# Kernel optimization log

Hardware: AMD Instinct MI355X
Metric: run time of the kernel (lower is better)

## Reference

```python
import jax, jax.numpy as jnp
import numpy as np

D_MODEL = 2048
NUM_HEADS = 16
HEAD_DIM = D_MODEL // NUM_HEADS
SCALE = 1.0 / np.sqrt(HEAD_DIM).astype(np.float32)
NEG_INF = -1e9


def setup_inputs() -> dict:
    key = jax.random.key(0)
    ks = jax.random.split(key, 10)
    B, S = 2, 2048
    x = jax.random.normal(ks[0], (B, S, D_MODEL), dtype=jnp.float32)
    # causal lower-triangular mask, broadcastable over (B, H)
    causal_mask = jnp.tril(jnp.ones((S, S), dtype=jnp.int32))[None, None]
    init = 1.0 / np.sqrt(D_MODEL)
    def lin(kw, kb):
        W = jax.random.uniform(kw, (D_MODEL, D_MODEL), jnp.float32, -init, init)
        b = jax.random.uniform(kb, (D_MODEL,), jnp.float32, -init, init)
        return W, b
    Wq, bq = lin(ks[1], ks[2])
    Wk, bk = lin(ks[3], ks[4])
    Wv, bv = lin(ks[5], ks[6])
    Wo, bo = lin(ks[7], ks[8])
    return {"x": x, "causal_mask": causal_mask,
            "Wq": Wq, "bq": bq, "Wk": Wk, "bk": bk,
            "Wv": Wv, "bv": bv, "Wo": Wo, "bo": bo}


def reference(x, causal_mask, Wq, bq, Wk, bk, Wv, bv, Wo, bo):
    B, S, _ = x.shape
    def proj(W, b):
        # torch Linear: x @ W.T + b -> (B, H, S, Dh)
        y = jnp.einsum('bsd,ed->bse', x, W) + b
        return y.reshape(B, S, NUM_HEADS, HEAD_DIM).transpose(0, 2, 1, 3)
    q = proj(Wq, bq)
    k = proj(Wk, bk)
    v = proj(Wv, bv)
    # apply_rope is a no-op stub in the source; q, k unchanged.
    scores = jnp.einsum('bhqd,bhkd->bhqk', q, k) * SCALE
    scores = jnp.where(causal_mask == 0, NEG_INF, scores)
    attn = jax.nn.softmax(scores, axis=-1)
    out = jnp.einsum('bhqk,bhkd->bhqd', attn, v)
    out = out.transpose(0, 2, 1, 3).reshape(B, S, D_MODEL)
    return jnp.einsum('bsd,ed->bse', out, Wo) + bo
```

## Files before the change

kernel.cpp:

```cpp
#include <hip/hip_runtime.h>
#include <hip/hip_bf16.h>
#include <stdint.h>
#include <stddef.h>

typedef __bf16 bf16_t;
typedef __bf16 bf16x4_t __attribute__((ext_vector_type(4)));
typedef __bf16 bf16x8_t __attribute__((ext_vector_type(8)));
typedef float f32x4 __attribute__((ext_vector_type(4)));

#define D_MODEL 2048
#define NHEADS 16
#define HDIM 128
#define SEQ 2048
#define BATCH 2
#define MTOT (BATCH * SEQ)
#define SCALE_F 0.08838834764831845f
#define LOG2E 1.4426950408889634f
#define QSCALE (SCALE_F * LOG2E)

#define AS1 __attribute__((address_space(1)))
#define AS3 __attribute__((address_space(3)))

__device__ __forceinline__ void load_lds16(const bf16_t* g, bf16_t* l) {
  __builtin_amdgcn_global_load_lds((AS1 void*)(g), (AS3 void*)(l), 16, 0, 0);
}

__global__ void cast_kernel(const float* __restrict__ src, bf16_t* __restrict__ dst, int n4) {
  int i = blockIdx.x * blockDim.x + threadIdx.x;
  if (i < n4) {
    float4 v = ((const float4*)src)[i];
    bf16x4_t o;
    o.x = (bf16_t)v.x; o.y = (bf16_t)v.y; o.z = (bf16_t)v.z; o.w = (bf16_t)v.w;
    ((bf16x4_t*)dst)[i] = o;
  }
}

__global__ void cast4_kernel(const float* __restrict__ s0, const float* __restrict__ s1,
                             const float* __restrict__ s2, const float* __restrict__ s3,
                             bf16_t* __restrict__ dst, int n4) {
  int i = blockIdx.x * blockDim.x + threadIdx.x;
  int y = blockIdx.y;
  if (i < n4) {
    const float* src = (y == 0) ? s0 : (y == 1) ? s1 : (y == 2) ? s2 : s3;
    float4 v = ((const float4*)src)[i];
    bf16x4_t o;
    o.x = (bf16_t)v.x; o.y = (bf16_t)v.y; o.z = (bf16_t)v.z; o.w = (bf16_t)v.w;
    ((bf16x4_t*)(dst + (size_t)y * D_MODEL * D_MODEL / 4 * 4))[i] = o;
  }
}

__global__ __launch_bounds__(256) void gemm_fused(
    const bf16_t* __restrict__ A, const bf16_t* __restrict__ Bm, int mode,
    const float* __restrict__ bias0, const float* __restrict__ bias1,
    const float* __restrict__ bias2,
    bf16_t* __restrict__ Qo, bf16_t* __restrict__ Ko, bf16_t* __restrict__ Vto,
    float* __restrict__ Out) {
  const int K = 2048;
  __shared__ __align__(16) bf16_t lA[128 * 64];
  __shared__ __align__(16) bf16_t lB[128 * 64];
  const int m0 = blockIdx.x * 128;
  const int n0 = blockIdx.y * 128;
  const int t = threadIdx.x;
  const int w = t >> 6, lane = t & 63;
  const int wm = w & 1, wn = w >> 1;
  const int la = lane & 15, lb = lane >> 4;

  f32x4 acc[4][4];
  f32x4 zero = {0.f, 0.f, 0.f, 0.f};
#pragma unroll
  for (int i = 0; i < 4; i++)
#pragma unroll
    for (int j = 0; j < 4; j++) acc[i][j] = zero;

  const int row0 = t >> 3, cc = t & 7;
  const int ccs = cc ^ (row0 & 7);
  const bf16_t* gA = A + (size_t)(m0 + row0) * K + ccs * 8;
  const bf16_t* gB = Bm + (size_t)(n0 + row0) * K + ccs * 8;
  bf16_t* sA = lA + t * 8;
  bf16_t* sB = lB + t * 8;

  for (int k0 = 0; k0 < K; k0 += 64) {
    __syncthreads();
#pragma unroll
    for (int i = 0; i < 4; i++)
      load_lds16(gA + k0 + (size_t)(32 * i) * K, sA + 2048 * i);
#pragma unroll
    for (int i = 0; i < 4; i++)
      load_lds16(gB + k0 + (size_t)(32 * i) * K, sB + 2048 * i);
    __syncthreads();
#pragma unroll
    for (int ks = 0; ks < 2; ks++) {
      bf16x8_t af[4], bfr[4];
#pragma unroll
      for (int mt = 0; mt < 4; mt++) {
        int row = wm * 64 + mt * 16 + la;
        af[mt] = *(const bf16x8_t*)(lA + row * 64 + (((ks * 4 + lb) ^ (la & 7)) * 8));
      }
#pragma unroll
      for (int nt = 0; nt < 4; nt++) {
        int row = wn * 64 + nt * 16 + la;
        bfr[nt] = *(const bf16x8_t*)(lB + row * 64 + (((ks * 4 + lb) ^ (la & 7)) * 8));
      }
#pragma unroll
      for (int mt = 0; mt < 4; mt++)
#pragma unroll
        for (int nt = 0; nt < 4; nt++)
          acc[mt][nt] = __builtin_amdgcn_mfma_f32_16x16x32_bf16(af[mt], bfr[nt], acc[mt][nt], 0, 0, 0);
    }
  }

  if (mode == 0) {
#pragma unroll
    for (int mt = 0; mt < 4; mt++) {
#pragma unroll
      for (int nt = 0; nt < 4; nt++) {
        int m = m0 + wm * 64 + mt * 16 + lb * 4;
        int n = n0 + wn * 64 + nt * 16 + la;
        int b = m >> 11, s = m & 2047;
        int which = n >> 11, hd = n & 2047;
        int h = hd >> 7, d = hd & 127;
        float bv = (which == 0 ? bias0 : which == 1 ? bias1 : bias2)[hd];
        f32x4 v = acc[mt][nt];
        if (which == 2) {
          bf16_t* dst = Vto + ((size_t)(b * NHEADS + h) * HDIM + d) * SEQ + s;
          bf16x4_t pk;
          pk.x = (bf16_t)(v.x + bv); pk.y = (bf16_t)(v.y + bv);
          pk.z = (bf16_t)(v.z + bv); pk.w = (bf16_t)(v.w + bv);
          *(bf16x4_t*)dst = pk;
        } else {
          float sc = (which == 0) ? QSCALE : 1.0f;
          bf16_t* dst = (which == 0 ? Qo : Ko) + ((size_t)(b * NHEADS + h) * SEQ + s) * HDIM + d;
          dst[0]        = (bf16_t)((v.x + bv) * sc);
          dst[HDIM]     = (bf16_t)((v.y + bv) * sc);
          dst[2 * HDIM] = (bf16_t)((v.z + bv) * sc);
          dst[3 * HDIM] = (bf16_t)((v.w + bv) * sc);
        }
      }
    }
  } else {
#pragma unroll
    for (int mt = 0; mt < 4; mt++) {
#pragma unroll
      for (int nt = 0; nt < 4; nt++) {
        int m = m0 + wm * 64 + mt * 16 + lb * 4;
        int n = n0 + wn * 64 + nt * 16 + la;
        float bv = bias0[n];
        f32x4 v = acc[mt][nt];
        float* dst = Out + (size_t)m * D_MODEL + n;
        dst[0]           = v.x + bv;
        dst[D_MODEL]     = v.y + bv;
        dst[2 * D_MODEL] = v.z + bv;
        dst[3 * D_MODEL] = v.w + bv;
      }
    }
  }
}

__global__ __launch_bounds__(256, 3) void flash_attn(
    const bf16_t* __restrict__ Q, const bf16_t* __restrict__ Kg,
    const bf16_t* __restrict__ Vt, bf16_t* __restrict__ O,
    bf16_t* __restrict__ PO, float* __restrict__ ML) {
  __shared__ __align__(16) bf16_t lK[64 * 128];
  __shared__ __align__(16) bf16_t lV[128 * 64];
  __shared__ __align__(16) bf16_t lP[128 * 72];
  const int g = blockIdx.x;
  const int piece = g >> 5, bh = g & 31;
  int qt, kt0, kt1, half;
  bool partial;
  if (piece < 16) {
    qt = 8 + (piece >> 1); half = piece & 1; partial = true;
    kt0 = half ? (qt + 1) : 0;
    kt1 = half ? (2 * qt + 2) : (qt + 1);
  } else {
    qt = piece - 16; half = 0; partial = false;
    kt0 = 0; kt1 = 2 * qt + 2;
  }
  const int q0 = qt * 128;
  const int t = threadIdx.x;
  const int w = t >> 6, lane = t & 63;
  const int la = lane & 15, lb = lane >> 4;
  const int qloc = w * 32 + la;

  const bf16_t* Qb = Q + (size_t)bh * SEQ * HDIM;
  const bf16_t* Kb = Kg + (size_t)bh * SEQ * HDIM;
  const bf16_t* Vb = Vt + (size_t)bh * HDIM * SEQ;

  bf16x8_t qf[2][4];
#pragma unroll
  for (int mt = 0; mt < 2; mt++)
#pragma unroll
    for (int ks = 0; ks < 4; ks++)
      qf[mt][ks] = *(const bf16x8_t*)(Qb + (size_t)(q0 + qloc + mt * 16) * HDIM + ks * 32 + lb * 8);

  f32x4 oacc[2][8];
  float mr[2] = {-3.0e38f, -3.0e38f}, lr[2] = {0.f, 0.f};
  f32x4 zero = {0.f, 0.f, 0.f, 0.f};
#pragma unroll
  for (int mt = 0; mt < 2; mt++)
#pragma unroll
    for (int dt = 0; dt < 8; dt++) oacc[mt][dt] = zero;

  for (int kt = kt0; kt < kt1; kt++) {
    const int j0 = kt * 64;
    __syncthreads();
#pragma unroll
    for (int i = 0; i < 4; i++) {
      int slot = t + 256 * i;
      int j = slot >> 4, cc = slot & 15;
      load_lds16(Kb + (size_t)(j0 + j) * HDIM + ((cc ^ (j & 15)) * 8), lK + slot * 8);
    }
#pragma unroll
    for (int i = 0; i < 4; i++) {
      int slot = t + 256 * i;
      int d = slot >> 3, jc = slot & 7;
      load_lds16(Vb + (size_t)d * SEQ + j0 + ((jc ^ (d & 7)) * 8), lV + slot * 8);
    }
    __syncthreads();

    f32x4 st[4][2];
#pragma unroll
    for (int nt = 0; nt < 4; nt++)
#pragma unroll
      for (int mt = 0; mt < 2; mt++) st[nt][mt] = zero;
#pragma unroll
    for (int ks = 0; ks < 4; ks++) {
#pragma unroll
      for (int nt = 0; nt < 4; nt++) {
        int j = nt * 16 + la;
        int cc = (lb + 4 * ks) ^ (j & 15);
        bf16x8_t kf = *(const bf16x8_t*)(lK + j * 128 + cc * 8);
#pragma unroll
        for (int mt = 0; mt < 2; mt++)
          st[nt][mt] = __builtin_amdgcn_mfma_f32_16x16x32_bf16(kf, qf[mt][ks], st[nt][mt], 0, 0, 0);
      }
    }

    const bool dm = (j0 + 64 > q0);
#pragma unroll
    for (int mt = 0; mt < 2; mt++) {
      int qg = q0 + qloc + mt * 16;
      if (dm) {
#pragma unroll
        for (int nt = 0; nt < 4; nt++)
#pragma unroll
          for (int r = 0; r < 4; r++)
            if (j0 + nt * 16 + lb * 4 + r > qg) st[nt][mt][r] = -3.0e38f;
      }
      float tm = -3.0e38f;
#pragma unroll
      for (int nt = 0; nt < 4; nt++)
#pragma unroll
        for (int r = 0; r < 4; r++) tm = fmaxf(tm, st[nt][mt][r]);
      tm = fmaxf(tm, __shfl_xor(tm, 16));
      tm = fmaxf(tm, __shfl_xor(tm, 32));
      float mnew = fmaxf(mr[mt], tm);
      float alpha = exp2f(mr[mt] - mnew);
      mr[mt] = mnew;
      lr[mt] *= alpha;
#pragma unroll
      for (int dt = 0; dt < 8; dt++) oacc[mt][dt] *= alpha;
      float s = 0.f;
#pragma unroll
      for (int nt = 0; nt < 4; nt++) {
        f32x4 p;
#pragma unroll
        for (int r = 0; r < 4; r++) {
          p[r] = exp2f(st[nt][mt][r] - mnew);
          s += p[r];
        }
        bf16x4_t pk;
        pk.x = (bf16_t)p[0]; pk.y = (bf16_t)p[1]; pk.z = (bf16_t)p[2]; pk.w = (bf16_t)p[3];
        *(bf16x4_t*)(lP + (qloc + mt * 16) * 72 + nt * 16 + lb * 4) = pk;
      }
      s += __shfl_xor(s, 16);
      s += __shfl_xor(s, 32);
      lr[mt] += s;
    }

    bf16x8_t pf[2][2];
#pragma unroll
    for (int mt = 0; mt < 2; mt++)
#pragma unroll
      for (int ks = 0; ks < 2; ks++)
        pf[mt][ks] = *(const bf16x8_t*)(lP + (qloc + mt * 16) * 72 + ks * 32 + lb * 8);
#pragma unroll
    for (int ks = 0; ks < 2; ks++) {
#pragma unroll
      for (int dt = 0; dt < 8; dt++) {
        int d = dt * 16 + la;
        int jc = (lb + 4 * ks) ^ (d & 7);
        bf16x8_t vf = *(const bf16x8_t*)(lV + d * 64 + jc * 8);
#pragma unroll
        for (int mt = 0; mt < 2; mt++)
          oacc[mt][dt] = __builtin_amdgcn_mfma_f32_16x16x32_bf16(vf, pf[mt][ks], oacc[mt][dt], 0, 0, 0);
      }
    }
  }

  if (!partial) {
    const int b = bh >> 4, h = bh & 15;
#pragma unroll
    for (int mt = 0; mt < 2; mt++) {
      float inv = 1.0f / lr[mt];
      int q = q0 + qloc + mt * 16;
      bf16_t* dst = O + ((size_t)b * SEQ + q) * D_MODEL + h * HDIM + lb * 4;
#pragma unroll
      for (int dt = 0; dt < 8; dt++) {
        f32x4 v = oacc[mt][dt];
        bf16x4_t pk;
        pk.x = (bf16_t)(v[0] * inv); pk.y = (bf16_t)(v[1] * inv);
        pk.z = (bf16_t)(v[2] * inv); pk.w = (bf16_t)(v[3] * inv);
        *(bf16x4_t*)(dst + dt * 16) = pk;
      }
    }
  } else {
    const int slot = ((qt - 8) * 32 + bh) * 2 + half;
    bf16_t* pob = PO + (size_t)slot * 128 * 128;
#pragma unroll
    for (int mt = 0; mt < 2; mt++) {
      int q = qloc + mt * 16;
      bf16_t* dst = pob + (size_t)q * 128 + lb * 4;
#pragma unroll
      for (int dt = 0; dt < 8; dt++) {
        f32x4 v = oacc[mt][dt];
        bf16x4_t pk;
        pk.x = (bf16_t)v[0]; pk.y = (bf16_t)v[1];
        pk.z = (bf16_t)v[2]; pk.w = (bf16_t)v[3];
        *(bf16x4_t*)(dst + dt * 16) = pk;
      }
      if (lb == 0) {
        float2 ml = make_float2(mr[mt], lr[mt]);
        *(float2*)(ML + ((size_t)slot * 128 + q) * 2) = ml;
      }
    }
  }
}

__global__ void merge_kernel(const bf16_t* __restrict__ PO, const float* __restrict__ ML,
                             bf16_t* __restrict__ O) {
  const int qti = blockIdx.x >> 5, bh = blockIdx.x & 31;
  const int qt = 8 + qti;
  const int t = threadIdx.x;
  const int q = t >> 1, dh = (t & 1) * 64;
  const size_t s1 = ((size_t)(qti * 32 + bh)) * 2;
  const float* ml1 = ML + (s1 * 128 + q) * 2;
  const float* ml2 = ML + ((s1 + 1) * 128 + q) * 2;
  float m1 = ml1[0], l1 = ml1[1], m2 = ml2[0], l2 = ml2[1];
  float m = fmaxf(m1, m2);
  float w1 = exp2f(m1 - m), w2 = exp2f(m2 - m);
  float inv = 1.0f / (w1 * l1 + w2 * l2);
  w1 *= inv; w2 *= inv;
  const bf16_t* p1 = PO + (s1 * 128 + q) * 128 + dh;
  const bf16_t* p2 = PO + ((s1 + 1) * 128 + q) * 128 + dh;
  const int b = bh >> 4, h = bh & 15;
  bf16_t* dst = O + ((size_t)b * SEQ + qt * 128 + q) * D_MODEL + h * HDIM + dh;
#pragma unroll
  for (int i = 0; i < 8; i++) {
    bf16x8_t a = ((const bf16x8_t*)p1)[i];
    bf16x8_t c = ((const bf16x8_t*)p2)[i];
    bf16x8_t o;
#pragma unroll
    for (int e = 0; e < 8; e++)
      o[e] = (bf16_t)(w1 * (float)a[e] + w2 * (float)c[e]);
    ((bf16x8_t*)dst)[i] = o;
  }
}

extern "C" void kernel_launch(void* const* d_in, const int* in_sizes, int n_in,
                              void* d_out, int out_size, void* d_ws, size_t ws_size,
                              hipStream_t stream) {
  (void)in_sizes; (void)n_in; (void)out_size; (void)ws_size;
  const float* x  = (const float*)d_in[0];
  const float* Wq = (const float*)d_in[2];
  const float* bq = (const float*)d_in[3];
  const float* Wk = (const float*)d_in[4];
  const float* bk = (const float*)d_in[5];
  const float* Wv = (const float*)d_in[6];
  const float* bv = (const float*)d_in[7];
  const float* Wo = (const float*)d_in[8];
  const float* bo = (const float*)d_in[9];
  float* out = (float*)d_out;

  const size_t NBF = (size_t)MTOT * D_MODEL * sizeof(bf16_t);
  const size_t WBF = (size_t)D_MODEL * D_MODEL * sizeof(bf16_t);
  char* p = (char*)d_ws;
  bf16_t* xb   = (bf16_t*)p; p += NBF;
  bf16_t* Wcat = (bf16_t*)p; p += 4 * WBF;
  bf16_t* Qb   = (bf16_t*)p; p += NBF;
  bf16_t* Kb   = (bf16_t*)p; p += NBF;
  bf16_t* Vtb  = (bf16_t*)p; p += NBF;
  bf16_t* Wob  = Wcat + (size_t)3 * D_MODEL * D_MODEL;
  bf16_t* Ob   = xb;
  bf16_t* PO = Wcat;
  float*  ML = (float*)(Wcat + (size_t)512 * 128 * 128);

  const int WN4 = D_MODEL * D_MODEL / 4;
  const int XN4 = MTOT * D_MODEL / 4;
  cast_kernel<<<XN4 / 256, 256, 0, stream>>>(x, xb, XN4);
  cast4_kernel<<<dim3(WN4 / 256, 4), 256, 0, stream>>>(Wq, Wk, Wv, Wo, Wcat, WN4);

  gemm_fused<<<dim3(MTOT / 128, 6144 / 128), 256, 0, stream>>>(
      xb, Wcat, 0, bq, bk, bv, Qb, Kb, Vtb, nullptr);

  flash_attn<<<dim3(768), 256, 0, stream>>>(Qb, Kb, Vtb, Ob, PO, ML);
  merge_kernel<<<dim3(256), 256, 0, stream>>>(PO, ML, Ob);

  gemm_fused<<<dim3(MTOT / 128, D_MODEL / 128), 256, 0, stream>>>(
      Ob, Wob, 1, bo, nullptr, nullptr, nullptr, nullptr, nullptr, out);
}
```

Measured before the change: 447.3 us.

## Double-buffer K/V tiles at 32 keys and pair causal work per block

The flash attention kernel now uses 32-key tiles and double-buffers K and V in shared memory, issuing the next tile's async global-to-LDS loads before computing on the current one. Work is rebalanced so that each block processes either one split half of a long query tile or a short query tile paired with the second half of a long one. This drops the grid from 768 to 512 blocks with more even per-block causal work. The intent is to hide load latency and reduce tail imbalance. The cost is extra barriers per key and a different LDS swizzle for V, and the initial max changes to -1e30.

```diff
diff --git a/kernel.cpp b/kernel.cpp
--- a/kernel.cpp
+++ b/kernel.cpp
@@ -17,6 +17,9 @@
 #define SCALE_F 0.08838834764831845f
 #define LOG2E 1.4426950408889634f
 #define QSCALE (SCALE_F * LOG2E)
+#define KT 32
+#define NEGI -3.0e38f
+#define MINIT -1.0e30f
 
 #define AS1 __attribute__((address_space(1)))
 #define AS3 __attribute__((address_space(3)))
@@ -160,22 +163,11 @@
     const bf16_t* __restrict__ Q, const bf16_t* __restrict__ Kg,
     const bf16_t* __restrict__ Vt, bf16_t* __restrict__ O,
     bf16_t* __restrict__ PO, float* __restrict__ ML) {
-  __shared__ __align__(16) bf16_t lK[64 * 128];
-  __shared__ __align__(16) bf16_t lV[128 * 64];
-  __shared__ __align__(16) bf16_t lP[128 * 72];
+  __shared__ __align__(16) bf16_t lK[2][KT * 128];
+  __shared__ __align__(16) bf16_t lV[2][128 * KT];
+  __shared__ __align__(16) bf16_t lP[128 * 40];
   const int g = blockIdx.x;
-  const int piece = g >> 5, bh = g & 31;
-  int qt, kt0, kt1, half;
-  bool partial;
-  if (piece < 16) {
-    qt = 8 + (piece >> 1); half = piece & 1; partial = true;
-    kt0 = half ? (qt + 1) : 0;
-    kt1 = half ? (2 * qt + 2) : (qt + 1);
-  } else {
-    qt = piece - 16; half = 0; partial = false;
-    kt0 = 0; kt1 = 2 * qt + 2;
-  }
-  const int q0 = qt * 128;
+  const int bh = g & 31, idx = g >> 5;
   const int t = threadIdx.x;
   const int w = t >> 6, lane = t & 63;
   const int la = lane & 15, lb = lane >> 4;
@@ -184,153 +176,192 @@
   const bf16_t* Qb = Q + (size_t)bh * SEQ * HDIM;
   const bf16_t* Kb = Kg + (size_t)bh * SEQ * HDIM;
   const bf16_t* Vb = Vt + (size_t)bh * HDIM * SEQ;
-
-  bf16x8_t qf[2][4];
-#pragma unroll
-  for (int mt = 0; mt < 2; mt++)
-#pragma unroll
-    for (int ks = 0; ks < 4; ks++)
-      qf[mt][ks] = *(const bf16x8_t*)(Qb + (size_t)(q0 + qloc + mt * 16) * HDIM + ks * 32 + lb * 8);
-
-  f32x4 oacc[2][8];
-  float mr[2] = {-3.0e38f, -3.0e38f}, lr[2] = {0.f, 0.f};
-  f32x4 zero = {0.f, 0.f, 0.f, 0.f};
-#pragma unroll
-  for (int mt = 0; mt < 2; mt++)
-#pragma unroll
-    for (int dt = 0; dt < 8; dt++) oacc[mt][dt] = zero;
-
-  for (int kt = kt0; kt < kt1; kt++) {
-    const int j0 = kt * 64;
+  const int b = bh >> 4, h = bh & 15;
+
+  int nph, qts[2], k0s[2], k1s[2], slots[2];
+  bool parts[2];
+  if (idx < 8) {
+    nph = 1; qts[0] = 8 + idx; k0s[0] = 0; k1s[0] = 34;
+    parts[0] = true; slots[0] = (idx * 32 + bh) * 2;
+  } else {
+    int qtA = idx - 8;
+    nph = 2;
+    qts[0] = qtA; k0s[0] = 0; k1s[0] = 4 * qtA + 4; parts[0] = false; slots[0] = 0;
+    qts[1] = 15 - qtA; k0s[1] = 34; k1s[1] = 64 - 4 * qtA;
+    parts[1] = true; slots[1] = ((7 - qtA) * 32 + bh) * 2 + 1;
+  }
+
+  const int kj = t >> 4, kcc = t & 15;
+  const int vd = t >> 2, vjc = t & 3;
+
+  for (int ph = 0; ph < nph; ph++) {
+    const int qt = qts[ph], kt0 = k0s[ph], kt1 = k1s[ph];
+    const int q0 = qt * 128;
+
+    bf16x8_t qf[2][4];
+#pragma unroll
+    for (int mt = 0; mt < 2; mt++)
+#pragma unroll
+      for (int ks = 0; ks < 4; ks++)
+        qf[mt][ks] = *(const bf16x8_t*)(Qb + (size_t)(q0 + qloc + mt * 16) * HDIM + ks * 32 + lb * 8);
+
+    f32x4 oacc[2][8];
+    float mr[2] = {MINIT, MINIT}, lr[2] = {0.f, 0.f};
+    f32x4 zero = {0.f, 0.f, 0.f, 0.f};
+#pragma unroll
+    for (int mt = 0; mt < 2; mt++)
+#pragma unroll
+      for (int dt = 0; dt < 8; dt++) oacc[mt][dt] = zero;
+
     __syncthreads();
-#pragma unroll
-    for (int i = 0; i < 4; i++) {
-      int slot = t + 256 * i;
-      int j = slot >> 4, cc = slot & 15;
-      load_lds16(Kb + (size_t)(j0 + j) * HDIM + ((cc ^ (j & 15)) * 8), lK + slot * 8);
-    }
-#pragma unroll
-    for (int i = 0; i < 4; i++) {
-      int slot = t + 256 * i;
-      int d = slot >> 3, jc = slot & 7;
-      load_lds16(Vb + (size_t)d * SEQ + j0 + ((jc ^ (d & 7)) * 8), lV + slot * 8);
-    }
-    __syncthreads();
-
-    f32x4 st[4][2];
-#pragma unroll
-    for (int nt = 0; nt < 4; nt++)
-#pragma unroll
-      for (int mt = 0; mt < 2; mt++) st[nt][mt] = zero;
-#pragma unroll
-    for (int ks = 0; ks < 4; ks++) {
-#pragma unroll
-      for (int nt = 0; nt < 4; nt++) {
-        int j = nt * 16 + la;
-        int cc = (lb + 4 * ks) ^ (j & 15);
-        bf16x8_t kf = *(const bf16x8_t*)(lK + j * 128 + cc * 8);
-#pragma unroll
-        for (int mt = 0; mt < 2; mt++)
-          st[nt][mt] = __builtin_amdgcn_mfma_f32_16x16x32_bf16(kf, qf[mt][ks], st[nt][mt], 0, 0, 0);
-      }
-    }
-
-    const bool dm = (j0 + 64 > q0);
-#pragma unroll
-    for (int mt = 0; mt < 2; mt++) {
-      int qg = q0 + qloc + mt * 16;
-      if (dm) {
-#pragma unroll
-        for (int nt = 0; nt < 4; nt++)
-#pragma unroll
-          for (int r = 0; r < 4; r++)
-            if (j0 + nt * 16 + lb * 4 + r > qg) st[nt][mt][r] = -3.0e38f;
-      }
-      float tm = -3.0e38f;
-#pragma unroll
-      for (int nt = 0; nt < 4; nt++)
-#pragma unroll
-        for (int r = 0; r < 4; r++) tm = fmaxf(tm, st[nt][mt][r]);
-      tm = fmaxf(tm, __shfl_xor(tm, 16));
-      tm = fmaxf(tm, __shfl_xor(tm, 32));
-      float mnew = fmaxf(mr[mt], tm);
-      float alpha = exp2f(mr[mt] - mnew);
-      mr[mt] = mnew;
-      lr[mt] *= alpha;
-#pragma unroll
-      for (int dt = 0; dt < 8; dt++) oacc[mt][dt] *= alpha;
-      float s = 0.f;
-#pragma unroll
-      for (int nt = 0; nt < 4; nt++) {
-        f32x4 p;
-#pragma unroll
-        for (int r = 0; r < 4; r++) {
-          p[r] = exp2f(st[nt][mt][r] - mnew);
-          s += p[r];
-        }
-        bf16x4_t pk;
-        pk.x = (bf16_t)p[0]; pk.y = (bf16_t)p[1]; pk.z = (bf16_t)p[2]; pk.w = (bf16_t)p[3];
-        *(bf16x4_t*)(lP + (qloc + mt * 16) * 72 + nt * 16 + lb * 4) = pk;
-      }
-      s += __shfl_xor(s, 16);
-      s += __shfl_xor(s, 32);
-      lr[mt] += s;
-    }
-
-    bf16x8_t pf[2][2];
-#pragma unroll
-    for (int mt = 0; mt < 2; mt++)
-#pragma unroll
-      for (int ks = 0; ks < 2; ks++)
-        pf[mt][ks] = *(const bf16x8_t*)(lP + (qloc + mt * 16) * 72 + ks * 32 + lb * 8);
-#pragma unroll
-    for (int ks = 0; ks < 2; ks++) {
+    {
+      const int j0 = kt0 * KT;
+      int buf = kt0 & 1;
+#pragma unroll
+      for (int i = 0; i < 2; i++) {
+        int j = kj + 16 * i;
+        load_lds16(Kb + (size_t)(j0 + j) * HDIM + (((kcc ^ (j & 15))) * 8),
+                   lK[buf] + (t + 256 * i) * 8);
+      }
+#pragma unroll
+      for (int i = 0; i < 2; i++) {
+        int d = vd + 64 * i;
+        load_lds16(Vb + (size_t)d * SEQ + j0 + (((vjc ^ ((d & 3) ^ ((d >> 2) & 3)))) * 8),
+                   lV[buf] + (t + 256 * i) * 8);
+      }
+    }
+
+    for (int kt = kt0; kt < kt1; kt++) {
+      const int j0 = kt * KT;
+      const int cur = kt & 1;
+      __syncthreads();
+
+      if (kt + 1 < kt1) {
+        const int jn = (kt + 1) * KT;
+        const int nb = cur ^ 1;
+#pragma unroll
+        for (int i = 0; i < 2; i++) {
+          int j = kj + 16 * i;
+          load_lds16(Kb + (size_t)(jn + j) * HDIM + (((kcc ^ (j & 15))) * 8),
+                     lK[nb] + (t + 256 * i) * 8);
+        }
+#pragma unroll
+        for (int i = 0; i < 2; i++) {
+          int d = vd + 64 * i;
+          load_lds16(Vb + (size_t)d * SEQ + jn + (((vjc ^ ((d & 3) ^ ((d >> 2) & 3)))) * 8),
+                     lV[nb] + (t + 256 * i) * 8);
+        }
+      }
+
+      f32x4 st[2][2];
+#pragma unroll
+      for (int nt = 0; nt < 2; nt++)
+#pragma unroll
+        for (int mt = 0; mt < 2; mt++) st[nt][mt] = zero;
+#pragma unroll
+      for (int ks = 0; ks < 4; ks++) {
+#pragma unroll
+        for (int nt = 0; nt < 2; nt++) {
+          int j = nt * 16 + la;
+          int ck = (ks * 4 + lb) ^ (j & 15);
+          bf16x8_t kf = *(const bf16x8_t*)(lK[cur] + j * 128 + ck * 8);
+#pragma unroll
+          for (int mt = 0; mt < 2; mt++)
+            st[nt][mt] = __builtin_amdgcn_mfma_f32_16x16x32_bf16(kf, qf[mt][ks], st[nt][mt], 0, 0, 0);
+        }
+      }
+
+      const bool dm = (j0 + KT > q0);
+#pragma unroll
+      for (int mt = 0; mt < 2; mt++) {
+        int qg = q0 + qloc + mt * 16;
+        if (dm) {
+#pragma unroll
+          for (int nt = 0; nt < 2; nt++)
+#pragma unroll
+            for (int r = 0; r < 4; r++)
+              if (j0 + nt * 16 + lb * 4 + r > qg) st[nt][mt][r] = NEGI;
+        }
+        float tm = NEGI;
+#pragma unroll
+        for (int nt = 0; nt < 2; nt++)
+#pragma unroll
+          for (int r = 0; r < 4; r++) tm = fmaxf(tm, st[nt][mt][r]);
+        tm = fmaxf(tm, __shfl_xor(tm, 16));
+        tm = fmaxf(tm, __shfl_xor(tm, 32));
+        float mnew = fmaxf(mr[mt], tm);
+        float alpha = exp2f(mr[mt] - mnew);
+        mr[mt] = mnew;
+        lr[mt] *= alpha;
+#pragma unroll
+        for (int dt = 0; dt < 8; dt++) oacc[mt][dt] *= alpha;
+        float s = 0.f;
+#pragma unroll
+        for (int nt = 0; nt < 2; nt++) {
+          f32x4 p;
+#pragma unroll
+          for (int r = 0; r < 4; r++) {
+            p[r] = exp2f(st[nt][mt][r] - mnew);
+            s += p[r];
+          }
+          bf16x4_t pk;
+          pk.x = (bf16_t)p[0]; pk.y = (bf16_t)p[1]; pk.z = (bf16_t)p[2]; pk.w = (bf16_t)p[3];
+          *(bf16x4_t*)(lP + (qloc + mt * 16) * 40 + nt * 16 + lb * 4) = pk;
+        }
+        s += __shfl_xor(s, 16);
+        s += __shfl_xor(s, 32);
+        lr[mt] += s;
+      }
+
+      bf16x8_t pf[2];
+#pragma unroll
+      for (int mt = 0; mt < 2; mt++)
+        pf[mt] = *(const bf16x8_t*)(lP + (w * 32 + mt * 16 + la) * 40 + lb * 8);
 #pragma unroll
       for (int dt = 0; dt < 8; dt++) {
         int d = dt * 16 + la;
-        int jc = (lb + 4 * ks) ^ (d & 7);
-        bf16x8_t vf = *(const bf16x8_t*)(lV + d * 64 + jc * 8);
+        int jc = lb ^ ((d & 3) ^ ((d >> 2) & 3));
+        bf16x8_t vf = *(const bf16x8_t*)(lV[cur] + d * 32 + jc * 8);
 #pragma unroll
         for (int mt = 0; mt < 2; mt++)
-          oacc[mt][dt] = __builtin_amdgcn_mfma_f32_16x16x32_bf16(vf, pf[mt][ks], oacc[mt][dt], 0, 0, 0);
-      }
-    }
-  }
-
-  if (!partial) {
-    const int b = bh >> 4, h = bh & 15;
-#pragma unroll
-    for (int mt = 0; mt < 2; mt++) {
-      float inv = 1.0f / lr[mt];
-      int q = q0 + qloc + mt * 16;
-      bf16_t* dst = O + ((size_t)b * SEQ + q) * D_MODEL + h * HDIM + lb * 4;
-#pragma unroll
-      for (int dt = 0; dt < 8; dt++) {
-        f32x4 v = oacc[mt][dt];
-        bf16x4_t pk;
-        pk.x = (bf16_t)(v[0] * inv); pk.y = (bf16_t)(v[1] * inv);
-        pk.z = (bf16_t)(v[2] * inv); pk.w = (bf16_t)(v[3] * inv);
-        *(bf16x4_t*)(dst + dt * 16) = pk;
-      }
-    }
-  } else {
-    const int slot = ((qt - 8) * 32 + bh) * 2 + half;
-    bf16_t* pob = PO + (size_t)slot * 128 * 128;
-#pragma unroll
-    for (int mt = 0; mt < 2; mt++) {
-      int q = qloc + mt * 16;
-      bf16_t* dst = pob + (size_t)q * 128 + lb * 4;
-#pragma unroll
-      for (int dt = 0; dt < 8; dt++) {
-        f32x4 v = oacc[mt][dt];
-        bf16x4_t pk;
-        pk.x = (bf16_t)v[0]; pk.y = (bf16_t)v[1];
-        pk.z = (bf16_t)v[2]; pk.w = (bf16_t)v[3];
-        *(bf16x4_t*)(dst + dt * 16) = pk;
-      }
-      if (lb == 0) {
-        float2 ml = make_float2(mr[mt], lr[mt]);
-        *(float2*)(ML + ((size_t)slot * 128 + q) * 2) = ml;
+          oacc[mt][dt] = __builtin_amdgcn_mfma_f32_16x16x32_bf16(vf, pf[mt], oacc[mt][dt], 0, 0, 0);
+      }
+    }
+
+    if (!parts[ph]) {
+#pragma unroll
+      for (int mt = 0; mt < 2; mt++) {
+        float inv = 1.0f / lr[mt];
+        int q = q0 + qloc + mt * 16;
+        bf16_t* dst = O + ((size_t)b * SEQ + q) * D_MODEL + h * HDIM + lb * 4;
+#pragma unroll
+        for (int dt = 0; dt < 8; dt++) {
+          f32x4 v = oacc[mt][dt];
+          bf16x4_t pk;
+          pk.x = (bf16_t)(v[0] * inv); pk.y = (bf16_t)(v[1] * inv);
+          pk.z = (bf16_t)(v[2] * inv); pk.w = (bf16_t)(v[3] * inv);
+          *(bf16x4_t*)(dst + dt * 16) = pk;
+        }
+      }
+    } else {
+      const int slot = slots[ph];
+      bf16_t* pob = PO + (size_t)slot * 128 * 128;
+#pragma unroll
+      for (int mt = 0; mt < 2; mt++) {
+        int q = qloc + mt * 16;
+        bf16_t* dst = pob + (size_t)q * 128 + lb * 4;
+#pragma unroll
+        for (int dt = 0; dt < 8; dt++) {
+          f32x4 v = oacc[mt][dt];
+          bf16x4_t pk;
+          pk.x = (bf16_t)v[0]; pk.y = (bf16_t)v[1];
+          pk.z = (bf16_t)v[2]; pk.w = (bf16_t)v[3];
+          *(bf16x4_t*)(dst + dt * 16) = pk;
+        }
+        if (lb == 0) {
+          float2 ml = make_float2(mr[mt], lr[mt]);
+          *(float2*)(ML + ((size_t)slot * 128 + q) * 2) = ml;
+        }
       }
     }
   }
@@ -402,7 +433,7 @@
   gemm_fused<<<dim3(MTOT / 128, 6144 / 128), 256, 0, stream>>>(
       xb, Wcat, 0, bq, bk, bv, Qb, Kb, Vtb, nullptr);
 
-  flash_attn<<<dim3(768), 256, 0, stream>>>(Qb, Kb, Vtb, Ob, PO, ML);
+  flash_attn<<<dim3(512), 256, 0, stream>>>(Qb, Kb, Vtb, Ob, PO, ML);
   merge_kernel<<<dim3(256), 256, 0, stream>>>(PO, ML, Ob);
 
   gemm_fused<<<dim3(MTOT / 128, D_MODEL / 128), 256, 0, stream>>>(
```

Result: faster. 405.9 us (-9.3%).
